# Performance work log

Measured on AMD Instinct MI355X. Metric: run time of the kernel, lower is better.

The kernel has to match this reference:

```python
import jax, jax.numpy as jnp
import numpy as np

B, C, H, W = 4, 256, 64, 64
C8 = C // 8  # query/key channel dim = in_dim // 8


def setup_inputs() -> dict:
    key = jax.random.key(0)
    ks = jax.random.split(key, 8)
    x = jax.random.normal(ks[0], (B, C, H, W), dtype=jnp.float32)
    # 1x1 convs == channel matmuls: weight [out_ch, in_ch], bias [out_ch]
    Wq = jax.random.normal(ks[1], (C8, C), dtype=jnp.float32) * (1.0 / np.sqrt(C))
    bq = jax.random.normal(ks[2], (C8,), dtype=jnp.float32) * 0.01
    Wk = jax.random.normal(ks[3], (C8, C), dtype=jnp.float32) * (1.0 / np.sqrt(C))
    bk = jax.random.normal(ks[4], (C8,), dtype=jnp.float32) * 0.01
    Wv = jax.random.normal(ks[5], (C, C), dtype=jnp.float32) * (1.0 / np.sqrt(C))
    bv = jax.random.normal(ks[6], (C,), dtype=jnp.float32) * 0.01
    gamma = jax.random.normal(ks[7], (1,), dtype=jnp.float32)
    return {"x": x, "Wq": Wq, "bq": bq, "Wk": Wk, "bk": bk, "Wv": Wv, "bv": bv, "gamma": gamma}


def reference(x, Wq, bq, Wk, bk, Wv, bv, gamma):
    b, c, h, w = x.shape
    n = h * w
    xf = x.reshape(b, c, n)                                    # [B, C, N]
    # 1x1 conv projections (channel matmuls + bias)
    q = jnp.einsum('dc,bcn->bnd', Wq, xf) + bq                 # [B, N, C8] (already permuted)
    k = jnp.einsum('dc,bcn->bdn', Wk, xf) + bk[:, None]        # [B, C8, N]
    v = jnp.einsum('dc,bcn->bdn', Wv, xf) + bv[:, None]        # [B, C,  N]
    S = jnp.einsum('bnd,bdm->bnm', q, k)                       # [B, N, N]
    # torch Softmax(dim=-2): normalize over the query/row axis n
    T = jax.nn.softmax(S, axis=-2)                             # attention_map_T
    # o = bmm(value, attention_map.permute(0,2,1)) = V @ T
    o = jnp.einsum('bcn,bnm->bcm', v, T).reshape(b, c, h, w)
    out = x + gamma * o
    attention_map = jnp.transpose(T, (0, 2, 1))
    return out, attention_map
```

## Files before the change

### kernel.cpp

```cpp
#include <hip/hip_runtime.h>

#define NN 4096
#define CC 256
#define CQ 32
#define BB 4

typedef _Float16 f16x8 __attribute__((ext_vector_type(8)));
typedef float    f32x4 __attribute__((ext_vector_type(4)));

__global__ __launch_bounds__(256) void qkv_proj(
    const float* __restrict__ x,
    const float* __restrict__ Wq, const float* __restrict__ bq,
    const float* __restrict__ Wk, const float* __restrict__ bk,
    const float* __restrict__ Wv, const float* __restrict__ bv,
    _Float16* __restrict__ qT, _Float16* __restrict__ kT,
    _Float16* __restrict__ vf)
{
    __shared__ float Wl[16 * 256];
    __shared__ float bl[16];
    const int t = threadIdx.x;
    const int g = blockIdx.y;
    const int b = blockIdx.z;
    const int n = blockIdx.x * 256 + t;

    const float* wsrc; const float* bsrc; int rowbase;
    if (g < 2)      { wsrc = Wq; bsrc = bq; rowbase = g * 16; }
    else if (g < 4) { wsrc = Wk; bsrc = bk; rowbase = (g - 2) * 16; }
    else            { wsrc = Wv; bsrc = bv; rowbase = (g - 4) * 16; }

    #pragma unroll
    for (int i = 0; i < 16; ++i) {
        int f = i * 256 + t;
        Wl[f] = wsrc[rowbase * 256 + f];
    }
    if (t < 16) bl[t] = bsrc[rowbase + t];
    __syncthreads();

    float acc[16];
    #pragma unroll
    for (int r = 0; r < 16; ++r) acc[r] = bl[r];

    const float* xp = x + ((size_t)b * CC) * NN + n;
    for (int c = 0; c < CC; ++c) {
        float xv = xp[(size_t)c * NN];
        #pragma unroll
        for (int r = 0; r < 16; ++r) acc[r] += Wl[r * 256 + c] * xv;
    }

    if (g < 4) {
        f16x8 h0, h1;
        #pragma unroll
        for (int r = 0; r < 8; ++r) { h0[r] = (_Float16)acc[r]; h1[r] = (_Float16)acc[8 + r]; }
        _Float16* dst = (g < 2) ? qT : kT;
        int half = (g < 2) ? g : (g - 2);
        size_t base = ((size_t)b * NN + n) * CQ + half * 16;
        *(f16x8*)&dst[base]     = h0;
        *(f16x8*)&dst[base + 8] = h1;
    } else {
        const int c0 = (g - 4) * 16;
        #pragma unroll
        for (int r = 0; r < 16; ++r)
            vf[((size_t)b * CC + c0 + r) * NN + n] = (_Float16)acc[r];
    }
}

__global__ __launch_bounds__(256) void attn_fused(
    const _Float16* __restrict__ qT, const _Float16* __restrict__ kT,
    const _Float16* __restrict__ vf, const float* __restrict__ x,
    const float* __restrict__ gamma,
    float* __restrict__ A, float* __restrict__ out)
{
    __shared__ __align__(16) _Float16 Pl[64 * 136];
    __shared__ float2 sred[4][64];
    __shared__ float2 sstat[64];

    const int t  = threadIdx.x;
    const int l  = t & 63, w = t >> 6;
    const int lr = l & 15, lg = l >> 4;
    const int m0 = blockIdx.x * 64;
    const int b  = blockIdx.y;

    f16x8 kf[4];
    #pragma unroll
    for (int g = 0; g < 4; ++g)
        kf[g] = *(const f16x8*)&kT[((size_t)b * NN + m0 + g * 16 + lr) * CQ + lg * 8];

    const _Float16* qb = qT + (size_t)b * NN * CQ;

    float mx[4][4], sm[4][4];
    #pragma unroll
    for (int g = 0; g < 4; ++g)
        #pragma unroll
        for (int r = 0; r < 4; ++r) { mx[g][r] = -1e30f; sm[g][r] = 0.0f; }

    for (int nt = 0; nt < NN / 128; ++nt) {
        f16x8 qf[2];
        #pragma unroll
        for (int h = 0; h < 2; ++h)
            qf[h] = *(const f16x8*)&qb[(size_t)(nt * 128 + w * 32 + h * 16 + lr) * CQ + lg * 8];
        #pragma unroll
        for (int g = 0; g < 4; ++g) {
            f32x4 s0 = (f32x4){0.f, 0.f, 0.f, 0.f};
            f32x4 s1 = (f32x4){0.f, 0.f, 0.f, 0.f};
            s0 = __builtin_amdgcn_mfma_f32_16x16x32_f16(kf[g], qf[0], s0, 0, 0, 0);
            s1 = __builtin_amdgcn_mfma_f32_16x16x32_f16(kf[g], qf[1], s1, 0, 0, 0);
            #pragma unroll
            for (int r = 0; r < 4; ++r) {
                float t0 = fmaxf(s0[r], s1[r]);
                float nm = fmaxf(mx[g][r], t0);
                float sadd = __expf(s0[r] - nm) + __expf(s1[r] - nm);
                sm[g][r] = sm[g][r] * __expf(mx[g][r] - nm) + sadd;
                mx[g][r] = nm;
            }
        }
    }

    #pragma unroll
    for (int off = 1; off < 16; off <<= 1)
        #pragma unroll
        for (int g = 0; g < 4; ++g)
            #pragma unroll
            for (int r = 0; r < 4; ++r) {
                float pm = __shfl_xor(mx[g][r], off, 64);
                float ps = __shfl_xor(sm[g][r], off, 64);
                float nm = fmaxf(mx[g][r], pm);
                sm[g][r] = sm[g][r] * __expf(mx[g][r] - nm) + ps * __expf(pm - nm);
                mx[g][r] = nm;
            }

    if (lr == 0) {
        #pragma unroll
        for (int g = 0; g < 4; ++g)
            #pragma unroll
            for (int r = 0; r < 4; ++r)
                sred[w][g * 16 + lg * 4 + r] = make_float2(mx[g][r], sm[g][r]);
    }
    __syncthreads();
    if (t < 64) {
        float2 a0 = sred[0][t], a1 = sred[1][t], a2 = sred[2][t], a3 = sred[3][t];
        float M = fmaxf(fmaxf(a0.x, a1.x), fmaxf(a2.x, a3.x));
        float S = a0.y * __expf(a0.x - M) + a1.y * __expf(a1.x - M)
                + a2.y * __expf(a2.x - M) + a3.y * __expf(a3.x - M);
        sstat[t] = make_float2(M, 1.0f / S);
    }
    __syncthreads();

    float2 stt[4][4];
    #pragma unroll
    for (int g = 0; g < 4; ++g)
        #pragma unroll
        for (int r = 0; r < 4; ++r)
            stt[g][r] = sstat[g * 16 + lg * 4 + r];

    f32x4 acc[4][4];
    #pragma unroll
    for (int g = 0; g < 4; ++g)
        #pragma unroll
        for (int h = 0; h < 4; ++h)
            acc[g][h] = (f32x4){0.f, 0.f, 0.f, 0.f};

    const _Float16* vb = vf + ((size_t)b * CC + w * 64) * NN;
    float* Ab = A + ((size_t)b * NN + m0) * NN;

    for (int nt = 0; nt < NN / 128; ++nt) {
        f16x8 qf[2];
        #pragma unroll
        for (int h = 0; h < 2; ++h)
            qf[h] = *(const f16x8*)&qb[(size_t)(nt * 128 + w * 32 + h * 16 + lr) * CQ + lg * 8];

        float p[4][2][4];
        #pragma unroll
        for (int g = 0; g < 4; ++g) {
            f32x4 s0 = (f32x4){0.f, 0.f, 0.f, 0.f};
            f32x4 s1 = (f32x4){0.f, 0.f, 0.f, 0.f};
            s0 = __builtin_amdgcn_mfma_f32_16x16x32_f16(kf[g], qf[0], s0, 0, 0, 0);
            s1 = __builtin_amdgcn_mfma_f32_16x16x32_f16(kf[g], qf[1], s1, 0, 0, 0);
            #pragma unroll
            for (int r = 0; r < 4; ++r) {
                p[g][0][r] = __expf(s0[r] - stt[g][r].x) * stt[g][r].y;
                p[g][1][r] = __expf(s1[r] - stt[g][r].x) * stt[g][r].y;
            }
        }

        __syncthreads();

        #pragma unroll
        for (int g = 0; g < 4; ++g)
            #pragma unroll
            for (int h = 0; h < 2; ++h)
                #pragma unroll
                for (int r = 0; r < 4; ++r) {
                    int m = g * 16 + lg * 4 + r;
                    int nc = w * 32 + h * 16 + lr;
                    Pl[m * 136 + nc] = (_Float16)p[g][h][r];
                }

        __syncthreads();

        #pragma unroll
        for (int g = 0; g < 4; ++g)
            #pragma unroll
            for (int h = 0; h < 2; ++h)
                #pragma unroll
                for (int r = 0; r < 4; ++r) {
                    int m = g * 16 + lg * 4 + r;
                    int nc = w * 32 + h * 16 + lr;
                    Ab[(size_t)m * NN + nt * 128 + nc] = p[g][h][r];
                }

        #pragma unroll
        for (int ks = 0; ks < 4; ++ks) {
            f16x8 vfr[4], pfr[4];
            #pragma unroll
            for (int g = 0; g < 4; ++g)
                vfr[g] = *(const f16x8*)&vb[(size_t)(g * 16 + lr) * NN + nt * 128 + ks * 32 + lg * 8];
            #pragma unroll
            for (int h = 0; h < 4; ++h)
                pfr[h] = *(const f16x8*)&Pl[(h * 16 + lr) * 136 + ks * 32 + lg * 8];
            #pragma unroll
            for (int g = 0; g < 4; ++g)
                #pragma unroll
                for (int h = 0; h < 4; ++h)
                    acc[g][h] = __builtin_amdgcn_mfma_f32_16x16x32_f16(
                        vfr[g], pfr[h], acc[g][h], 0, 0, 0);
        }
    }

    const float gm = gamma[0];
    #pragma unroll
    for (int g = 0; g < 4; ++g) {
        #pragma unroll
        for (int r = 0; r < 4; ++r) {
            int c = w * 64 + g * 16 + lg * 4 + r;
            size_t ro = ((size_t)b * CC + c) * NN + m0;
            #pragma unroll
            for (int h = 0; h < 4; ++h) {
                int m = h * 16 + lr;
                out[ro + m] = x[ro + m] + gm * acc[g][h][r];
            }
        }
    }
}

extern "C" void kernel_launch(void* const* d_in, const int* in_sizes, int n_in,
                              void* d_out, int out_size, void* d_ws, size_t ws_size,
                              hipStream_t stream) {
    const float* x     = (const float*)d_in[0];
    const float* Wq    = (const float*)d_in[1];
    const float* bq    = (const float*)d_in[2];
    const float* Wk    = (const float*)d_in[3];
    const float* bk    = (const float*)d_in[4];
    const float* Wv    = (const float*)d_in[5];
    const float* bv    = (const float*)d_in[6];
    const float* gamma = (const float*)d_in[7];

    float* out = (float*)d_out;
    float* A   = out + (size_t)BB * CC * NN;

    _Float16* qT = (_Float16*)d_ws;
    _Float16* kT = qT + (size_t)BB * NN * CQ;
    _Float16* vf = kT + (size_t)BB * NN * CQ;

    qkv_proj  <<<dim3(NN / 256, 20, BB), 256, 0, stream>>>(x, Wq, bq, Wk, bk, Wv, bv, qT, kT, vf);
    attn_fused<<<dim3(NN / 64, BB),      256, 0, stream>>>(qT, kT, vf, x, gamma, A, out);
}
```

Baseline: 497.4 us.

## Halve attention row tile, swizzle block order, prefetch Q, reorder A stores

The attention kernel now processes 32 key rows per block instead of 64, doubling the grid to 512 blocks, and asks for two blocks per CU. Blocks are remapped with an XCD-style swizzle. Q fragments are software-prefetched one tile ahead, and the attention-map stores are issued before the barrier. The projection kernel drops its LDS weight staging in favour of direct (broadcast) global loads with the channel loop unrolled by 4. Smaller tiles raise parallelism and occupancy, but each block re-reads V and Q twice as often relative to its output.

```diff
diff --git a/kernel.cpp b/kernel.cpp
--- a/kernel.cpp
+++ b/kernel.cpp
@@ -4,6 +4,7 @@
 #define CC 256
 #define CQ 32
 #define BB 4
+#define MT 32
 
 typedef _Float16 f16x8 __attribute__((ext_vector_type(8)));
 typedef float    f32x4 __attribute__((ext_vector_type(4)));
@@ -16,8 +17,6 @@
     _Float16* __restrict__ qT, _Float16* __restrict__ kT,
     _Float16* __restrict__ vf)
 {
-    __shared__ float Wl[16 * 256];
-    __shared__ float bl[16];
     const int t = threadIdx.x;
     const int g = blockIdx.y;
     const int b = blockIdx.z;
@@ -28,23 +27,22 @@
     else if (g < 4) { wsrc = Wk; bsrc = bk; rowbase = (g - 2) * 16; }
     else            { wsrc = Wv; bsrc = bv; rowbase = (g - 4) * 16; }
 
-    #pragma unroll
-    for (int i = 0; i < 16; ++i) {
-        int f = i * 256 + t;
-        Wl[f] = wsrc[rowbase * 256 + f];
-    }
-    if (t < 16) bl[t] = bsrc[rowbase + t];
-    __syncthreads();
+    const float* Wr = wsrc + rowbase * 256;
 
     float acc[16];
     #pragma unroll
-    for (int r = 0; r < 16; ++r) acc[r] = bl[r];
+    for (int r = 0; r < 16; ++r) acc[r] = bsrc[rowbase + r];
 
     const float* xp = x + ((size_t)b * CC) * NN + n;
-    for (int c = 0; c < CC; ++c) {
-        float xv = xp[(size_t)c * NN];
-        #pragma unroll
-        for (int r = 0; r < 16; ++r) acc[r] += Wl[r * 256 + c] * xv;
+    for (int c = 0; c < CC; c += 4) {
+        float xv0 = xp[(size_t)(c + 0) * NN];
+        float xv1 = xp[(size_t)(c + 1) * NN];
+        float xv2 = xp[(size_t)(c + 2) * NN];
+        float xv3 = xp[(size_t)(c + 3) * NN];
+        #pragma unroll
+        for (int r = 0; r < 16; ++r)
+            acc[r] += Wr[r * 256 + c] * xv0 + Wr[r * 256 + c + 1] * xv1
+                    + Wr[r * 256 + c + 2] * xv2 + Wr[r * 256 + c + 3] * xv3;
     }
 
     if (g < 4) {
@@ -64,42 +62,52 @@
     }
 }
 
-__global__ __launch_bounds__(256) void attn_fused(
+__global__ __launch_bounds__(256, 2) void attn_fused(
     const _Float16* __restrict__ qT, const _Float16* __restrict__ kT,
     const _Float16* __restrict__ vf, const float* __restrict__ x,
     const float* __restrict__ gamma,
     float* __restrict__ A, float* __restrict__ out)
 {
-    __shared__ __align__(16) _Float16 Pl[64 * 136];
-    __shared__ float2 sred[4][64];
-    __shared__ float2 sstat[64];
+    __shared__ __align__(16) _Float16 Pl[MT * 136];
+    __shared__ float2 sred[4][MT];
+    __shared__ float2 sstat[MT];
 
     const int t  = threadIdx.x;
     const int l  = t & 63, w = t >> 6;
     const int lr = l & 15, lg = l >> 4;
-    const int m0 = blockIdx.x * 64;
-    const int b  = blockIdx.y;
-
-    f16x8 kf[4];
-    #pragma unroll
-    for (int g = 0; g < 4; ++g)
+
+    const int flat  = blockIdx.y * (NN / MT) + blockIdx.x;
+    const int work  = (flat & 7) * (BB * NN / MT / 8) + (flat >> 3);
+    const int b     = work / (NN / MT);
+    const int m0    = (work % (NN / MT)) * MT;
+
+    f16x8 kf[2];
+    #pragma unroll
+    for (int g = 0; g < 2; ++g)
         kf[g] = *(const f16x8*)&kT[((size_t)b * NN + m0 + g * 16 + lr) * CQ + lg * 8];
 
     const _Float16* qb = qT + (size_t)b * NN * CQ;
 
-    float mx[4][4], sm[4][4];
-    #pragma unroll
-    for (int g = 0; g < 4; ++g)
+    float mx[2][4], sm[2][4];
+    #pragma unroll
+    for (int g = 0; g < 2; ++g)
         #pragma unroll
         for (int r = 0; r < 4; ++r) { mx[g][r] = -1e30f; sm[g][r] = 0.0f; }
 
+    f16x8 qf[2];
+    #pragma unroll
+    for (int h = 0; h < 2; ++h)
+        qf[h] = *(const f16x8*)&qb[(size_t)(w * 32 + h * 16 + lr) * CQ + lg * 8];
+
     for (int nt = 0; nt < NN / 128; ++nt) {
-        f16x8 qf[2];
+        const int ntn = (nt + 1) & (NN / 128 - 1);
+        f16x8 qn[2];
         #pragma unroll
         for (int h = 0; h < 2; ++h)
-            qf[h] = *(const f16x8*)&qb[(size_t)(nt * 128 + w * 32 + h * 16 + lr) * CQ + lg * 8];
-        #pragma unroll
-        for (int g = 0; g < 4; ++g) {
+            qn[h] = *(const f16x8*)&qb[(size_t)(ntn * 128 + w * 32 + h * 16 + lr) * CQ + lg * 8];
+
+        #pragma unroll
+        for (int g = 0; g < 2; ++g) {
             f32x4 s0 = (f32x4){0.f, 0.f, 0.f, 0.f};
             f32x4 s1 = (f32x4){0.f, 0.f, 0.f, 0.f};
             s0 = __builtin_amdgcn_mfma_f32_16x16x32_f16(kf[g], qf[0], s0, 0, 0, 0);
@@ -113,12 +121,13 @@
                 mx[g][r] = nm;
             }
         }
+        qf[0] = qn[0]; qf[1] = qn[1];
     }
 
     #pragma unroll
     for (int off = 1; off < 16; off <<= 1)
         #pragma unroll
-        for (int g = 0; g < 4; ++g)
+        for (int g = 0; g < 2; ++g)
             #pragma unroll
             for (int r = 0; r < 4; ++r) {
                 float pm = __shfl_xor(mx[g][r], off, 64);
@@ -130,13 +139,13 @@
 
     if (lr == 0) {
         #pragma unroll
-        for (int g = 0; g < 4; ++g)
+        for (int g = 0; g < 2; ++g)
             #pragma unroll
             for (int r = 0; r < 4; ++r)
                 sred[w][g * 16 + lg * 4 + r] = make_float2(mx[g][r], sm[g][r]);
     }
     __syncthreads();
-    if (t < 64) {
+    if (t < MT) {
         float2 a0 = sred[0][t], a1 = sred[1][t], a2 = sred[2][t], a3 = sred[3][t];
         float M = fmaxf(fmaxf(a0.x, a1.x), fmaxf(a2.x, a3.x));
         float S = a0.y * __expf(a0.x - M) + a1.y * __expf(a1.x - M)
@@ -145,32 +154,32 @@
     }
     __syncthreads();
 
-    float2 stt[4][4];
-    #pragma unroll
-    for (int g = 0; g < 4; ++g)
+    float2 stt[2][4];
+    #pragma unroll
+    for (int g = 0; g < 2; ++g)
         #pragma unroll
         for (int r = 0; r < 4; ++r)
             stt[g][r] = sstat[g * 16 + lg * 4 + r];
 
-    f32x4 acc[4][4];
+    f32x4 acc[4][2];
     #pragma unroll
     for (int g = 0; g < 4; ++g)
         #pragma unroll
-        for (int h = 0; h < 4; ++h)
+        for (int h = 0; h < 2; ++h)
             acc[g][h] = (f32x4){0.f, 0.f, 0.f, 0.f};
 
     const _Float16* vb = vf + ((size_t)b * CC + w * 64) * NN;
     float* Ab = A + ((size_t)b * NN + m0) * NN;
 
+    #pragma unroll
+    for (int h = 0; h < 2; ++h)
+        qf[h] = *(const f16x8*)&qb[(size_t)(w * 32 + h * 16 + lr) * CQ + lg * 8];
+
+    #pragma unroll 1
     for (int nt = 0; nt < NN / 128; ++nt) {
-        f16x8 qf[2];
-        #pragma unroll
-        for (int h = 0; h < 2; ++h)
-            qf[h] = *(const f16x8*)&qb[(size_t)(nt * 128 + w * 32 + h * 16 + lr) * CQ + lg * 8];
-
-        float p[4][2][4];
-        #pragma unroll
-        for (int g = 0; g < 4; ++g) {
+        float p[2][2][4];
+        #pragma unroll
+        for (int g = 0; g < 2; ++g) {
             f32x4 s0 = (f32x4){0.f, 0.f, 0.f, 0.f};
             f32x4 s1 = (f32x4){0.f, 0.f, 0.f, 0.f};
             s0 = __builtin_amdgcn_mfma_f32_16x16x32_f16(kf[g], qf[0], s0, 0, 0, 0);
@@ -182,10 +191,27 @@
             }
         }
 
+        #pragma unroll
+        for (int g = 0; g < 2; ++g)
+            #pragma unroll
+            for (int h = 0; h < 2; ++h)
+                #pragma unroll
+                for (int r = 0; r < 4; ++r) {
+                    int m = g * 16 + lg * 4 + r;
+                    int nc = w * 32 + h * 16 + lr;
+                    Ab[(size_t)m * NN + nt * 128 + nc] = p[g][h][r];
+                }
+
+        const int ntn = (nt + 1) & (NN / 128 - 1);
+        f16x8 qn[2];
+        #pragma unroll
+        for (int h = 0; h < 2; ++h)
+            qn[h] = *(const f16x8*)&qb[(size_t)(ntn * 128 + w * 32 + h * 16 + lr) * CQ + lg * 8];
+
         __syncthreads();
 
         #pragma unroll
-        for (int g = 0; g < 4; ++g)
+        for (int g = 0; g < 2; ++g)
             #pragma unroll
             for (int h = 0; h < 2; ++h)
                 #pragma unroll
@@ -198,32 +224,22 @@
         __syncthreads();
 
         #pragma unroll
-        for (int g = 0; g < 4; ++g)
-            #pragma unroll
-            for (int h = 0; h < 2; ++h)
-                #pragma unroll
-                for (int r = 0; r < 4; ++r) {
-                    int m = g * 16 + lg * 4 + r;
-                    int nc = w * 32 + h * 16 + lr;
-                    Ab[(size_t)m * NN + nt * 128 + nc] = p[g][h][r];
-                }
-
-        #pragma unroll
         for (int ks = 0; ks < 4; ++ks) {
-            f16x8 vfr[4], pfr[4];
+            f16x8 vfr[4], pfr[2];
             #pragma unroll
             for (int g = 0; g < 4; ++g)
                 vfr[g] = *(const f16x8*)&vb[(size_t)(g * 16 + lr) * NN + nt * 128 + ks * 32 + lg * 8];
             #pragma unroll
-            for (int h = 0; h < 4; ++h)
+            for (int h = 0; h < 2; ++h)
                 pfr[h] = *(const f16x8*)&Pl[(h * 16 + lr) * 136 + ks * 32 + lg * 8];
             #pragma unroll
             for (int g = 0; g < 4; ++g)
                 #pragma unroll
-                for (int h = 0; h < 4; ++h)
+                for (int h = 0; h < 2; ++h)
                     acc[g][h] = __builtin_amdgcn_mfma_f32_16x16x32_f16(
                         vfr[g], pfr[h], acc[g][h], 0, 0, 0);
         }
+        qf[0] = qn[0]; qf[1] = qn[1];
     }
 
     const float gm = gamma[0];
@@ -234,7 +250,7 @@
             int c = w * 64 + g * 16 + lg * 4 + r;
             size_t ro = ((size_t)b * CC + c) * NN + m0;
             #pragma unroll
-            for (int h = 0; h < 4; ++h) {
+            for (int h = 0; h < 2; ++h) {
                 int m = h * 16 + lr;
                 out[ro + m] = x[ro + m] + gm * acc[g][h][r];
             }
@@ -262,5 +278,5 @@
     _Float16* vf = kT + (size_t)BB * NN * CQ;
 
     qkv_proj  <<<dim3(NN / 256, 20, BB), 256, 0, stream>>>(x, Wq, bq, Wk, bk, Wv, bv, qT, kT, vf);
-    attn_fused<<<dim3(NN / 64, BB),      256, 0, stream>>>(qT, kT, vf, x, gamma, A, out);
+    attn_fused<<<dim3(NN / MT, BB),      256, 0, stream>>>(qT, kT, vf, x, gamma, A, out);
 }
```

Result: no change. 499.7 us (+0.5%).

## Double-buffer P tile, prefetch Q, nontemporal stores, restructure QKV projection

Applied to the files above, without the earlier changes.

The attention kernel now double-buffers the shared P tile so one barrier per iteration replaces two, and prefetches the next Q fragments while the current tile is being processed. It writes the attention map and output with nontemporal stores and remaps blocks so consecutive blocks land on different XCD groups. The projection kernel now computes 64 output rows per thread, reading weights directly from global/scalar memory instead of staging them in LDS, which cuts the number of x re-reads. This raises register pressure, and launch_bounds(256,2) may force spills.

```diff
diff --git a/kernel.cpp b/kernel.cpp
--- a/kernel.cpp
+++ b/kernel.cpp
@@ -4,11 +4,14 @@
 #define CC 256
 #define CQ 32
 #define BB 4
+#define MT 64
+#define PLSTR 136
+#define PLSZ (MT * PLSTR)
 
 typedef _Float16 f16x8 __attribute__((ext_vector_type(8)));
 typedef float    f32x4 __attribute__((ext_vector_type(4)));
 
-__global__ __launch_bounds__(256) void qkv_proj(
+__global__ __launch_bounds__(128) void qkv_proj(
     const float* __restrict__ x,
     const float* __restrict__ Wq, const float* __restrict__ bq,
     const float* __restrict__ Wk, const float* __restrict__ bk,
@@ -16,69 +19,81 @@
     _Float16* __restrict__ qT, _Float16* __restrict__ kT,
     _Float16* __restrict__ vf)
 {
-    __shared__ float Wl[16 * 256];
-    __shared__ float bl[16];
     const int t = threadIdx.x;
     const int g = blockIdx.y;
     const int b = blockIdx.z;
-    const int n = blockIdx.x * 256 + t;
-
-    const float* wsrc; const float* bsrc; int rowbase;
-    if (g < 2)      { wsrc = Wq; bsrc = bq; rowbase = g * 16; }
-    else if (g < 4) { wsrc = Wk; bsrc = bk; rowbase = (g - 2) * 16; }
-    else            { wsrc = Wv; bsrc = bv; rowbase = (g - 4) * 16; }
-
-    #pragma unroll
-    for (int i = 0; i < 16; ++i) {
-        int f = i * 256 + t;
-        Wl[f] = wsrc[rowbase * 256 + f];
-    }
-    if (t < 16) bl[t] = bsrc[rowbase + t];
-    __syncthreads();
-
-    float acc[16];
-    #pragma unroll
-    for (int r = 0; r < 16; ++r) acc[r] = bl[r];
+    const int n = blockIdx.x * 128 + t;
+
+    const float *W0, *W1, *b0, *b1;
+    if (g == 0) { W0 = Wq; W1 = Wk; b0 = bq; b1 = bk; }
+    else {
+        W0 = Wv + (size_t)(g - 1) * 64 * 256;
+        W1 = W0 + 32 * 256;
+        b0 = bv + (g - 1) * 64;
+        b1 = b0 + 32;
+    }
+
+    float acc[64];
+    #pragma unroll
+    for (int r = 0; r < 32; ++r) { acc[r] = b0[r]; acc[32 + r] = b1[r]; }
 
     const float* xp = x + ((size_t)b * CC) * NN + n;
-    for (int c = 0; c < CC; ++c) {
-        float xv = xp[(size_t)c * NN];
-        #pragma unroll
-        for (int r = 0; r < 16; ++r) acc[r] += Wl[r * 256 + c] * xv;
-    }
-
-    if (g < 4) {
-        f16x8 h0, h1;
-        #pragma unroll
-        for (int r = 0; r < 8; ++r) { h0[r] = (_Float16)acc[r]; h1[r] = (_Float16)acc[8 + r]; }
-        _Float16* dst = (g < 2) ? qT : kT;
-        int half = (g < 2) ? g : (g - 2);
-        size_t base = ((size_t)b * NN + n) * CQ + half * 16;
-        *(f16x8*)&dst[base]     = h0;
-        *(f16x8*)&dst[base + 8] = h1;
+    for (int c = 0; c < CC; c += 4) {
+        float xv0 = xp[(size_t)(c + 0) * NN];
+        float xv1 = xp[(size_t)(c + 1) * NN];
+        float xv2 = xp[(size_t)(c + 2) * NN];
+        float xv3 = xp[(size_t)(c + 3) * NN];
+        #pragma unroll
+        for (int r = 0; r < 32; ++r)
+            acc[r] += W0[r * 256 + c] * xv0 + W0[r * 256 + c + 1] * xv1
+                    + W0[r * 256 + c + 2] * xv2 + W0[r * 256 + c + 3] * xv3;
+        #pragma unroll
+        for (int r = 0; r < 32; ++r)
+            acc[32 + r] += W1[r * 256 + c] * xv0 + W1[r * 256 + c + 1] * xv1
+                         + W1[r * 256 + c + 2] * xv2 + W1[r * 256 + c + 3] * xv3;
+    }
+
+    if (g == 0) {
+        size_t base = ((size_t)b * NN + n) * CQ;
+        #pragma unroll
+        for (int j = 0; j < 4; ++j) {
+            f16x8 hq, hk;
+            #pragma unroll
+            for (int r = 0; r < 8; ++r) {
+                hq[r] = (_Float16)acc[j * 8 + r];
+                hk[r] = (_Float16)acc[32 + j * 8 + r];
+            }
+            *(f16x8*)&qT[base + j * 8] = hq;
+            *(f16x8*)&kT[base + j * 8] = hk;
+        }
     } else {
-        const int c0 = (g - 4) * 16;
-        #pragma unroll
-        for (int r = 0; r < 16; ++r)
-            vf[((size_t)b * CC + c0 + r) * NN + n] = (_Float16)acc[r];
+        const int c0 = (g - 1) * 64;
+        #pragma unroll
+        for (int r = 0; r < 32; ++r) {
+            vf[((size_t)b * CC + c0 + r) * NN + n]      = (_Float16)acc[r];
+            vf[((size_t)b * CC + c0 + 32 + r) * NN + n] = (_Float16)acc[32 + r];
+        }
     }
 }
 
-__global__ __launch_bounds__(256) void attn_fused(
+__global__ __launch_bounds__(256, 2) void attn_fused(
     const _Float16* __restrict__ qT, const _Float16* __restrict__ kT,
     const _Float16* __restrict__ vf, const float* __restrict__ x,
     const float* __restrict__ gamma,
     float* __restrict__ A, float* __restrict__ out)
 {
-    __shared__ __align__(16) _Float16 Pl[64 * 136];
-    __shared__ float2 sred[4][64];
-    __shared__ float2 sstat[64];
+    __shared__ __align__(16) _Float16 Pl[2 * PLSZ];
+    __shared__ float2 sred[4][MT];
+    __shared__ float sM[MT], sR[MT];
 
     const int t  = threadIdx.x;
     const int l  = t & 63, w = t >> 6;
     const int lr = l & 15, lg = l >> 4;
-    const int m0 = blockIdx.x * 64;
-    const int b  = blockIdx.y;
+
+    const int flat = blockIdx.y * (NN / MT) + blockIdx.x;
+    const int work = (flat & 7) * (BB * NN / MT / 8) + (flat >> 3);
+    const int b    = work / (NN / MT);
+    const int m0   = (work % (NN / MT)) * MT;
 
     f16x8 kf[4];
     #pragma unroll
@@ -93,11 +108,18 @@
         #pragma unroll
         for (int r = 0; r < 4; ++r) { mx[g][r] = -1e30f; sm[g][r] = 0.0f; }
 
+    f16x8 qf[2];
+    #pragma unroll
+    for (int h = 0; h < 2; ++h)
+        qf[h] = *(const f16x8*)&qb[(size_t)(w * 32 + h * 16 + lr) * CQ + lg * 8];
+
     for (int nt = 0; nt < NN / 128; ++nt) {
-        f16x8 qf[2];
+        const int ntn = (nt + 1) & (NN / 128 - 1);
+        f16x8 qn[2];
         #pragma unroll
         for (int h = 0; h < 2; ++h)
-            qf[h] = *(const f16x8*)&qb[(size_t)(nt * 128 + w * 32 + h * 16 + lr) * CQ + lg * 8];
+            qn[h] = *(const f16x8*)&qb[(size_t)(ntn * 128 + w * 32 + h * 16 + lr) * CQ + lg * 8];
+
         #pragma unroll
         for (int g = 0; g < 4; ++g) {
             f32x4 s0 = (f32x4){0.f, 0.f, 0.f, 0.f};
@@ -113,6 +135,7 @@
                 mx[g][r] = nm;
             }
         }
+        qf[0] = qn[0]; qf[1] = qn[1];
     }
 
     #pragma unroll
@@ -136,21 +159,14 @@
                 sred[w][g * 16 + lg * 4 + r] = make_float2(mx[g][r], sm[g][r]);
     }
     __syncthreads();
-    if (t < 64) {
+    if (t < MT) {
         float2 a0 = sred[0][t], a1 = sred[1][t], a2 = sred[2][t], a3 = sred[3][t];
         float M = fmaxf(fmaxf(a0.x, a1.x), fmaxf(a2.x, a3.x));
         float S = a0.y * __expf(a0.x - M) + a1.y * __expf(a1.x - M)
                 + a2.y * __expf(a2.x - M) + a3.y * __expf(a3.x - M);
-        sstat[t] = make_float2(M, 1.0f / S);
+        sM[t] = M; sR[t] = 1.0f / S;
     }
     __syncthreads();
-
-    float2 stt[4][4];
-    #pragma unroll
-    for (int g = 0; g < 4; ++g)
-        #pragma unroll
-        for (int r = 0; r < 4; ++r)
-            stt[g][r] = sstat[g * 16 + lg * 4 + r];
 
     f32x4 acc[4][4];
     #pragma unroll
@@ -162,51 +178,41 @@
     const _Float16* vb = vf + ((size_t)b * CC + w * 64) * NN;
     float* Ab = A + ((size_t)b * NN + m0) * NN;
 
+    #pragma unroll
+    for (int h = 0; h < 2; ++h)
+        qf[h] = *(const f16x8*)&qb[(size_t)(w * 32 + h * 16 + lr) * CQ + lg * 8];
+
+    #pragma unroll 2
     for (int nt = 0; nt < NN / 128; ++nt) {
-        f16x8 qf[2];
-        #pragma unroll
-        for (int h = 0; h < 2; ++h)
-            qf[h] = *(const f16x8*)&qb[(size_t)(nt * 128 + w * 32 + h * 16 + lr) * CQ + lg * 8];
-
-        float p[4][2][4];
+        _Float16* Plb = &Pl[(nt & 1) * PLSZ];
+
         #pragma unroll
         for (int g = 0; g < 4; ++g) {
             f32x4 s0 = (f32x4){0.f, 0.f, 0.f, 0.f};
             f32x4 s1 = (f32x4){0.f, 0.f, 0.f, 0.f};
             s0 = __builtin_amdgcn_mfma_f32_16x16x32_f16(kf[g], qf[0], s0, 0, 0, 0);
             s1 = __builtin_amdgcn_mfma_f32_16x16x32_f16(kf[g], qf[1], s1, 0, 0, 0);
+            f32x4 Mv = *(const f32x4*)&sM[g * 16 + lg * 4];
+            f32x4 Rv = *(const f32x4*)&sR[g * 16 + lg * 4];
             #pragma unroll
             for (int r = 0; r < 4; ++r) {
-                p[g][0][r] = __expf(s0[r] - stt[g][r].x) * stt[g][r].y;
-                p[g][1][r] = __expf(s1[r] - stt[g][r].x) * stt[g][r].y;
-            }
-        }
-
-        __syncthreads();
-
-        #pragma unroll
-        for (int g = 0; g < 4; ++g)
-            #pragma unroll
-            for (int h = 0; h < 2; ++h)
-                #pragma unroll
-                for (int r = 0; r < 4; ++r) {
-                    int m = g * 16 + lg * 4 + r;
-                    int nc = w * 32 + h * 16 + lr;
-                    Pl[m * 136 + nc] = (_Float16)p[g][h][r];
-                }
-
-        __syncthreads();
-
-        #pragma unroll
-        for (int g = 0; g < 4; ++g)
-            #pragma unroll
-            for (int h = 0; h < 2; ++h)
-                #pragma unroll
-                for (int r = 0; r < 4; ++r) {
-                    int m = g * 16 + lg * 4 + r;
-                    int nc = w * 32 + h * 16 + lr;
-                    Ab[(size_t)m * NN + nt * 128 + nc] = p[g][h][r];
-                }
+                float p0 = __expf(s0[r] - Mv[r]) * Rv[r];
+                float p1 = __expf(s1[r] - Mv[r]) * Rv[r];
+                int m   = g * 16 + lg * 4 + r;
+                int nc0 = w * 32 + lr, nc1 = nc0 + 16;
+                __builtin_nontemporal_store(p0, &Ab[(size_t)m * NN + nt * 128 + nc0]);
+                __builtin_nontemporal_store(p1, &Ab[(size_t)m * NN + nt * 128 + nc1]);
+                Plb[m * PLSTR + nc0] = (_Float16)p0;
+                Plb[m * PLSTR + nc1] = (_Float16)p1;
+            }
+        }
+
+        const int ntn = (nt + 1) & (NN / 128 - 1);
+        f16x8 qn0 = *(const f16x8*)&qb[(size_t)(ntn * 128 + w * 32 + lr) * CQ + lg * 8];
+        f16x8 qn1 = *(const f16x8*)&qb[(size_t)(ntn * 128 + w * 32 + 16 + lr) * CQ + lg * 8];
+
+        asm volatile("s_waitcnt lgkmcnt(0)" ::: "memory");
+        __builtin_amdgcn_s_barrier();
 
         #pragma unroll
         for (int ks = 0; ks < 4; ++ks) {
@@ -216,7 +222,7 @@
                 vfr[g] = *(const f16x8*)&vb[(size_t)(g * 16 + lr) * NN + nt * 128 + ks * 32 + lg * 8];
             #pragma unroll
             for (int h = 0; h < 4; ++h)
-                pfr[h] = *(const f16x8*)&Pl[(h * 16 + lr) * 136 + ks * 32 + lg * 8];
+                pfr[h] = *(const f16x8*)&Plb[(h * 16 + lr) * PLSTR + ks * 32 + lg * 8];
             #pragma unroll
             for (int g = 0; g < 4; ++g)
                 #pragma unroll
@@ -224,6 +230,7 @@
                     acc[g][h] = __builtin_amdgcn_mfma_f32_16x16x32_f16(
                         vfr[g], pfr[h], acc[g][h], 0, 0, 0);
         }
+        qf[0] = qn0; qf[1] = qn1;
     }
 
     const float gm = gamma[0];
@@ -236,7 +243,7 @@
             #pragma unroll
             for (int h = 0; h < 4; ++h) {
                 int m = h * 16 + lr;
-                out[ro + m] = x[ro + m] + gm * acc[g][h][r];
+                __builtin_nontemporal_store(x[ro + m] + gm * acc[g][h][r], &out[ro + m]);
             }
         }
     }
@@ -261,6 +268,6 @@
     _Float16* kT = qT + (size_t)BB * NN * CQ;
     _Float16* vf = kT + (size_t)BB * NN * CQ;
 
-    qkv_proj  <<<dim3(NN / 256, 20, BB), 256, 0, stream>>>(x, Wq, bq, Wk, bk, Wv, bv, qT, kT, vf);
-    attn_fused<<<dim3(NN / 64, BB),      256, 0, stream>>>(qT, kT, vf, x, gamma, A, out);
+    qkv_proj  <<<dim3(NN / 128, 5, BB), 128, 0, stream>>>(x, Wq, bq, Wk, bk, Wv, bv, qT, kT, vf);
+    attn_fused<<<dim3(NN / MT, BB),     256, 0, stream>>>(qT, kT, vf, x, gamma, A, out);
 }
```

Result: slower. 642.9 us (+29.3%).
